# Kernel optimization log

Hardware: AMD Instinct MI355X
Metric: run time of the kernel (lower is better)

The kernel has to match this reference:

```python
import jax, jax.numpy as jnp
import numpy as np

G = 4096              # number of graphs in batch
NPG = 198             # nodes per graph (fixed by view(-1, 198*2))
N = G * NPG           # total nodes = 811008
DEG = 8               # avg degree
E = N * DEG           # total edges = 6488064
CONV_DIMS = [(2, 20), (20, 15), (15, 10), (10, 5), (5, 2)]
MLP_DIMS = [(396, 200), (200, 100), (100, 50), (50, 10), (10, 2)]


def setup_inputs() -> dict:
    key = jax.random.key(0)
    ks = jax.random.split(key, 64)
    x = jax.random.normal(ks[0], (N, 2), dtype=jnp.float32)
    # block-diagonal edges: endpoints within each 198-node graph, then offset
    src = jax.random.randint(ks[1], (G, E // G), 0, NPG)
    dst = jax.random.randint(ks[2], (G, E // G), 0, NPG)
    off = (jnp.arange(G, dtype=jnp.int32) * NPG)[:, None]
    edge_index = jnp.stack([(src + off).reshape(-1), (dst + off).reshape(-1)]).astype(jnp.int32)
    edge_weight = jax.random.uniform(ks[3], (E,), dtype=jnp.float32)
    inp = {"x": x, "edge_index": edge_index, "edge_weight": edge_weight}
    ki = 4
    for i, (ci, co) in enumerate(CONV_DIMS):
        s = 1.0 / np.sqrt(ci)
        inp[f"w_rel{i}"] = jax.random.normal(ks[ki], (co, ci), jnp.float32) * s; ki += 1
        inp[f"b_rel{i}"] = jax.random.normal(ks[ki], (co,), jnp.float32) * s; ki += 1
        inp[f"w_root{i}"] = jax.random.normal(ks[ki], (co, ci), jnp.float32) * s; ki += 1
    for i, (ci, co) in enumerate(MLP_DIMS):
        s = 1.0 / np.sqrt(ci)
        inp[f"lw{i}"] = jax.random.normal(ks[ki], (co, ci), jnp.float32) * s; ki += 1
        inp[f"lb{i}"] = jax.random.normal(ks[ki], (co,), jnp.float32) * s; ki += 1
    return inp


def _graph_conv(x, src, dst, ew, w_rel, b_rel, w_root):
    # PyG GraphConv: lin_rel(sum_{j->i} e_ji * x_j) + lin_root(x_i)
    msg = x[src] * ew[:, None]                               # [E, Cin] gather
    agg = jax.ops.segment_sum(msg, dst, num_segments=N)      # [N, Cin] scatter-add
    return agg @ w_rel.T + b_rel + x @ w_root.T              # [N, Cout]


def reference(x, edge_index, edge_weight,
              w_rel0, b_rel0, w_root0, w_rel1, b_rel1, w_root1,
              w_rel2, b_rel2, w_root2, w_rel3, b_rel3, w_root3,
              w_rel4, b_rel4, w_root4,
              lw0, lb0, lw1, lb1, lw2, lb2, lw3, lb3, lw4, lb4):
    src, dst = edge_index[0], edge_index[1]
    convs = [(w_rel0, b_rel0, w_root0), (w_rel1, b_rel1, w_root1),
             (w_rel2, b_rel2, w_root2), (w_rel3, b_rel3, w_root3),
             (w_rel4, b_rel4, w_root4)]
    h = x
    for wr, br, wroot in convs:
        h = jax.nn.relu(_graph_conv(h, src, dst, edge_weight, wr, br, wroot))
    h = h.reshape(-1, NPG * 2)                               # [G, 396]
    mlp = [(lw0, lb0), (lw1, lb1), (lw2, lb2), (lw3, lb3)]
    for w, b in mlp:
        h = jax.nn.relu(h @ w.T + b)
    logits = h @ lw4.T + lb4                                 # [G, 2]
    return jax.nn.softmax(logits, axis=1)
```

## Files before the change

### kernel.cpp

```cpp
#include <hip/hip_runtime.h>
#include <hip/hip_fp16.h>

#define NG    4096
#define NPG   198
#define EPG   1584
#define ETOT  (NG * EPG)
#define SWW   14

#define BC2(u) __builtin_bit_cast(__half2, (u))

typedef _Float16 f16x4 __attribute__((ext_vector_type(4)));
typedef float    f32x4 __attribute__((ext_vector_type(4)));
typedef float    f32x2 __attribute__((ext_vector_type(2)));

#define H_F16S    (NG * 396)
#define WTB_SZ    114688
#define WTB1_OFF  83200
#define WTB2_OFF  106496
#define WTB3_OFF  113664
#define CPK_PAIRS 562

__global__ __launch_bounds__(256) void wpack_kernel(
    const float* __restrict__ w0, const float* __restrict__ w1,
    const float* __restrict__ w2, const float* __restrict__ w3,
    const float* wr0, const float* wq0, const float* wr1, const float* wq1,
    const float* wr2, const float* wq2, const float* wr3, const float* wq3,
    const float* wr4, const float* wq4,
    _Float16* __restrict__ wtb, f32x2* __restrict__ cpk)
{
    const int idx = blockIdx.x * 256 + threadIdx.x;
    if (idx < 2 * WTB_SZ) {
        const int half = idx >= WTB_SZ;
        const int rel0 = idx - half * WTB_SZ;
        const float* w; int K, N, NPAD, rel;
        if (rel0 < 83200)       { w = w0; K = 396; N = 200; NPAD = 208; rel = rel0; }
        else if (rel0 < 106496) { w = w1; K = 200; N = 100; NPAD = 112; rel = rel0 - 83200; }
        else if (rel0 < 113664) { w = w2; K = 100; N = 50;  NPAD = 64;  rel = rel0 - 106496; }
        else                    { w = w3; K = 50;  N = 10;  NPAD = 16;  rel = rel0 - 113664; }
        const int span = NPAD * 16;
        const int kc = rel / span;
        const int r  = rel - kc * span;
        const int n  = r >> 4, ki = r & 15;
        const int k  = kc * 16 + ki;
        const float v = (n < N && k < K) ? w[n * K + k] : 0.f;
        const _Float16 hi = (_Float16)v;
        wtb[idx] = half ? (_Float16)(v - (float)hi) : hi;
        return;
    }
    const int cidx = idx - 2 * WTB_SZ;
    if (cidx >= CPK_PAIRS) return;
    const float *wrel, *wroot; int COUT, CIN, MSP, base;
    if (cidx < 40)       { wrel=wr0; wroot=wq0; COUT=20; CIN=2;  MSP=1;  base=0;   }
    else if (cidx < 340) { wrel=wr1; wroot=wq1; COUT=15; CIN=20; MSP=10; base=40;  }
    else if (cidx < 500) { wrel=wr2; wroot=wq2; COUT=10; CIN=15; MSP=8;  base=340; }
    else if (cidx < 550) { wrel=wr3; wroot=wq3; COUT=5;  CIN=10; MSP=5;  base=500; }
    else                 { wrel=wr4; wroot=wq4; COUT=2;  CIN=5;  MSP=3;  base=550; }
    const int r    = cidx - base;
    const int half = r >= COUT * MSP;
    const int q    = r - half * COUT * MSP;
    const int o    = q / MSP, p = q - o * MSP;
    const float* w = half ? wroot : wrel;
    const int c0 = 2 * p, c1 = 2 * p + 1;
    f32x2 v;
    v.x = (c0 < CIN) ? w[o * CIN + c0] : 0.f;
    v.y = (c1 < CIN) ? w[o * CIN + c1] : 0.f;
    cpk[cidx] = v;
}

template <int CIN, int COUT, int SIN, int SOUT>
__device__ __forceinline__ void conv_layer_h(
    const unsigned* __restrict__ h_in,
    unsigned* __restrict__ h_out,
    const unsigned* __restrict__ s_edge,
    const unsigned short* __restrict__ row_start,
    const unsigned short* __restrict__ perm,
    const f32x2* __restrict__ wrelp,
    const f32x2* __restrict__ wrootp,
    const float* __restrict__ brel, int tid)
{
    if (tid >= NPG) return;
    const int node = (int)perm[tid];
    constexpr int MS = (CIN + 1) / 2;

    float aggf[MS * 2];
#pragma unroll
    for (int c = 0; c < MS * 2; ++c) aggf[c] = 0.f;

    const unsigned jb = row_start[node], je = row_start[node + 1];
    for (unsigned j = jb; j < je; ++j) {
        const unsigned e  = s_edge[j];
        const float    wf = __half2float(__ushort_as_half((unsigned short)(e >> 16)));
        const unsigned* row = h_in + (e & 0xFFFFu) * SIN;
        unsigned wv[MS];
        if constexpr (SIN == 1) {
            wv[0] = row[0];
        } else {
#pragma unroll
            for (int p = 0; p + 1 < MS; p += 2) {
                const uint2 q = *(const uint2*)(row + p);
                wv[p] = q.x; wv[p + 1] = q.y;
            }
            if constexpr (MS & 1) wv[MS - 1] = row[MS - 1];
        }
#pragma unroll
        for (int p = 0; p < MS; ++p) {
            const __half2 h2 = BC2(wv[p]);
            aggf[2*p]     = fmaf(wf, __low2float(h2),  aggf[2*p]);
            aggf[2*p + 1] = fmaf(wf, __high2float(h2), aggf[2*p + 1]);
        }
    }

    float hv[MS * 2];
    {
        const unsigned* me = h_in + node * SIN;
        unsigned mw[MS];
        if constexpr (SIN == 1) {
            mw[0] = me[0];
        } else {
#pragma unroll
            for (int p = 0; p + 1 < MS; p += 2) {
                const uint2 q = *(const uint2*)(me + p);
                mw[p] = q.x; mw[p + 1] = q.y;
            }
            if constexpr (MS & 1) mw[MS - 1] = me[MS - 1];
        }
#pragma unroll
        for (int p = 0; p < MS; ++p) {
            const __half2 h2 = BC2(mw[p]);
            hv[2*p]     = __low2float(h2);
            hv[2*p + 1] = __high2float(h2);
        }
    }

    float outv[COUT];
#pragma unroll
    for (int o = 0; o < COUT; ++o) {
        f32x2 acc; acc.x = brel[o]; acc.y = 0.f;
#pragma unroll
        for (int p = 0; p < MS; ++p) {
            f32x2 av; av.x = aggf[2*p]; av.y = aggf[2*p+1];
            acc = __builtin_elementwise_fma(av, wrelp[o * MS + p], acc);
            f32x2 hv2; hv2.x = hv[2*p]; hv2.y = hv[2*p+1];
            acc = __builtin_elementwise_fma(hv2, wrootp[o * MS + p], acc);
        }
        outv[o] = fmaxf(acc.x + acc.y, 0.f);
    }

    if constexpr (SOUT == 1) {
        h_out[node] = __builtin_bit_cast(unsigned,
            __floats2half2_rn(outv[0], COUT > 1 ? outv[1] : 0.f));
    } else {
        unsigned ow[SOUT];
#pragma unroll
        for (int p = 0; p < SOUT; ++p) {
            const float lo = (2 * p     < COUT) ? outv[2 * p]     : 0.f;
            const float hi = (2 * p + 1 < COUT) ? outv[2 * p + 1] : 0.f;
            ow[p] = __builtin_bit_cast(unsigned, __floats2half2_rn(lo, hi));
        }
        unsigned* orow = h_out + node * SOUT;
#pragma unroll
        for (int qn = 0; qn < SOUT; qn += 2)
            *(uint2*)(orow + qn) = make_uint2(ow[qn], ow[qn + 1]);
    }
}

__global__ __launch_bounds__(256) void conv_kernel(
    const float* __restrict__ x,
    const int*   __restrict__ eidx,
    const float* __restrict__ ew,
    const f32x2* __restrict__ cpk,
    const float* __restrict__ br0, const float* __restrict__ br1,
    const float* __restrict__ br2, const float* __restrict__ br3,
    const float* __restrict__ br4,
    _Float16* __restrict__ H)
{
    __shared__ __align__(16) unsigned s_edge[EPG];
    __shared__ unsigned       cnt[256];
    __shared__ unsigned short row_start[NPG + 2];
    __shared__ unsigned       wsum[4];
    __shared__ unsigned       dhist[64];
    __shared__ unsigned       dcur[64];
    __shared__ unsigned short perm[NPG + 2];
    __shared__ __align__(16) unsigned bufA[NPG * SWW];
    __shared__ __align__(16) unsigned bufB[NPG * SWW];

    const int g = blockIdx.x, tid = threadIdx.x;
    const int ebase = g * EPG, nbase = g * NPG;
    const int lane = tid & 63, wid = tid >> 6;

    const int4*   s4 = (const int4*)(eidx + ebase);
    const int4*   d4 = (const int4*)(eidx + ETOT + ebase);
    const float4* w4 = (const float4*)(ew + ebase);
    const int4   sa = s4[tid];
    const int4   da = d4[tid];
    const float4 wa = w4[tid];
    const bool hasb = tid < (EPG / 4 - 256);
    int4 sb = {0,0,0,0}, db = {0,0,0,0}; float4 wb = {0,0,0,0};
    if (hasb) { sb = s4[tid + 256]; db = d4[tid + 256]; wb = w4[tid + 256]; }

    cnt[tid] = 0u;
    __syncthreads();
    atomicAdd(&cnt[da.x - nbase], 1u); atomicAdd(&cnt[da.y - nbase], 1u);
    atomicAdd(&cnt[da.z - nbase], 1u); atomicAdd(&cnt[da.w - nbase], 1u);
    if (hasb) {
        atomicAdd(&cnt[db.x - nbase], 1u); atomicAdd(&cnt[db.y - nbase], 1u);
        atomicAdd(&cnt[db.z - nbase], 1u); atomicAdd(&cnt[db.w - nbase], 1u);
    }
    __syncthreads();

    const unsigned v = cnt[tid];
    unsigned inc = v;
#pragma unroll
    for (int s = 1; s < 64; s <<= 1) {
        const unsigned t = (unsigned)__shfl_up((int)inc, s);
        if (lane >= s) inc += t;
    }
    if (lane == 63) wsum[wid] = inc;
    __syncthreads();
    unsigned pre = 0;
    for (int w = 0; w < wid; ++w) pre += wsum[w];
    const unsigned excl = pre + inc - v;
    if (tid <= NPG) row_start[tid] = (unsigned short)excl;
    cnt[tid] = excl;
    __syncthreads();

    {
        auto place = [&](int s, int d, float w) {
            const int dl = d - nbase;
            const unsigned slot = atomicAdd(&cnt[dl], 1u);
            const __half hw = __float2half_rn(w);
            s_edge[slot] = ((unsigned)__half_as_ushort(hw) << 16)
                         | (unsigned)(s - nbase);
        };
        place(sa.x, da.x, wa.x); place(sa.y, da.y, wa.y);
        place(sa.z, da.z, wa.z); place(sa.w, da.w, wa.w);
        if (hasb) {
            place(sb.x, db.x, wb.x); place(sb.y, db.y, wb.y);
            place(sb.z, db.z, wb.z); place(sb.w, db.w, wb.w);
        }
    }

    if (tid < NPG) {
        const float2 xv = ((const float2*)x)[nbase + tid];
        bufA[tid] = __builtin_bit_cast(unsigned, __floats2half2_rn(xv.x, xv.y));
    }

    if (tid < 64) dhist[tid] = 0u;
    __syncthreads();
    unsigned mydeg = 0u;
    if (tid < NPG) {
        mydeg = v; if (mydeg > 63u) mydeg = 63u;
        atomicAdd(&dhist[mydeg], 1u);
    }
    __syncthreads();
    if (tid < 64) {
        const unsigned dv = dhist[tid];
        unsigned sc = dv;
#pragma unroll
        for (int s = 1; s < 64; s <<= 1) {
            const unsigned t = (unsigned)__shfl_up((int)sc, s);
            if (lane >= s) sc += t;
        }
        dcur[tid] = sc - dv;
    }
    __syncthreads();
    if (tid < NPG) {
        const unsigned pos = atomicAdd(&dcur[mydeg], 1u);
        perm[pos] = (unsigned short)tid;
    }
    __syncthreads();

    conv_layer_h<2,  20, 1,   SWW>(bufA, bufB, s_edge, row_start, perm,
                                   cpk + 0,   cpk + 20,        br0, tid);
    __syncthreads();
    conv_layer_h<20, 15, SWW, SWW>(bufB, bufA, s_edge, row_start, perm,
                                   cpk + 40,  cpk + 40 + 150,  br1, tid);
    __syncthreads();
    conv_layer_h<15, 10, SWW, SWW>(bufA, bufB, s_edge, row_start, perm,
                                   cpk + 340, cpk + 340 + 80,  br2, tid);
    __syncthreads();
    conv_layer_h<10, 5,  SWW, SWW>(bufB, bufA, s_edge, row_start, perm,
                                   cpk + 500, cpk + 500 + 25,  br3, tid);
    __syncthreads();
    conv_layer_h<5,  2,  SWW, 1  >(bufA, bufB, s_edge, row_start, perm,
                                   cpk + 550, cpk + 550 + 6,   br4, tid);
    __syncthreads();

    if (tid < NPG)
        ((unsigned*)H)[g * NPG + tid] = bufB[tid];
}

__device__ __forceinline__ void zero_words(void* p, int nwords, int tid)
{
    unsigned* u = (unsigned*)p;
    for (int i = tid; i < nwords; i += 512) u[i] = 0u;
}

template<int KC, int NTT, int NOUT, int SIN, int SOUT>
__device__ __forceinline__ void mfma_layer(
    const _Float16* __restrict__ inb,
    _Float16* __restrict__ outb,
    const _Float16* __restrict__ wthi,
    const _Float16* __restrict__ wtlo,
    const float* __restrict__ bias, int tid)
{
    constexpr int NPAD = NTT * 16;
    const int lane = tid & 63, wid = tid >> 6;
    const int lrow = lane & 15, lgrp = lane >> 4;
    const int nt0 = wid;
    if (nt0 >= NTT) return;
    const bool has2 = (nt0 + 8) < NTT;
    const _Float16* aptr = inb + lrow * SIN + lgrp * 4;

    f32x4 acc0 = {0.f, 0.f, 0.f, 0.f};
    f32x4 acc1 = {0.f, 0.f, 0.f, 0.f};
    const int n0 = nt0 * 16 + lrow;
    const int n1 = (nt0 + 8) * 16 + lrow;
    const int boff0 = n0 * 16 + lgrp * 4;
    const int boff1 = n1 * 16 + lgrp * 4;
#pragma unroll 4
    for (int kc = 0; kc < KC; ++kc) {
        const f16x4 a = *(const f16x4*)(aptr + kc * 16);
        const size_t kb = (size_t)kc * (NPAD * 16);
        acc0 = __builtin_amdgcn_mfma_f32_16x16x16f16(
            a, *(const f16x4*)(wthi + kb + boff0), acc0, 0, 0, 0);
        acc0 = __builtin_amdgcn_mfma_f32_16x16x16f16(
            a, *(const f16x4*)(wtlo + kb + boff0), acc0, 0, 0, 0);
        if (has2) {
            acc1 = __builtin_amdgcn_mfma_f32_16x16x16f16(
                a, *(const f16x4*)(wthi + kb + boff1), acc1, 0, 0, 0);
            acc1 = __builtin_amdgcn_mfma_f32_16x16x16f16(
                a, *(const f16x4*)(wtlo + kb + boff1), acc1, 0, 0, 0);
        }
    }
    if (n0 < NOUT) {
        const float bv = bias[n0];
#pragma unroll
        for (int j = 0; j < 4; ++j)
            outb[(lgrp * 4 + j) * SOUT + n0] = (_Float16)fmaxf(acc0[j] + bv, 0.f);
    }
    if (has2 && n1 < NOUT) {
        const float bv = bias[n1];
#pragma unroll
        for (int j = 0; j < 4; ++j)
            outb[(lgrp * 4 + j) * SOUT + n1] = (_Float16)fmaxf(acc1[j] + bv, 0.f);
    }
}

__global__ __launch_bounds__(512) void mlp_mfma_kernel(
    const _Float16* __restrict__ H,
    const _Float16* __restrict__ wtb,
    const float* __restrict__ lb0, const float* __restrict__ lb1,
    const float* __restrict__ lb2, const float* __restrict__ lb3,
    const float* __restrict__ lw4, const float* __restrict__ lb4,
    float* __restrict__ out)
{
    __shared__ __align__(16) _Float16 bufH[16 * 400];
    __shared__ __align__(16) _Float16 bufX[16 * 224];
    __shared__ __align__(16) _Float16 bufY[16 * 128];

    const int tid   = threadIdx.x;
    const int gbase = blockIdx.x * 8;
    const _Float16* lo = wtb + WTB_SZ;

    {
        const unsigned* Hw = (const unsigned*)H + (size_t)gbase * 198;
        unsigned* bH = (unsigned*)bufH;
        for (int t = tid; t < 16 * 200; t += 512) {
            const int gg = t / 200, w = t - gg * 200;
            bH[gg * 200 + w] = (gg < 8 && w < 198) ? Hw[gg * 198 + w] : 0u;
        }
        zero_words(bufX, 16 * 224 / 2, tid);
        zero_words(bufY, 16 * 128 / 2, tid);
    }
    __syncthreads();

    mfma_layer<25, 13, 200, 400, 224>(bufH, bufX, wtb, lo, lb0, tid);
    __syncthreads();

    zero_words(bufH, 512, tid);
    mfma_layer<13, 7, 100, 224, 128>(bufX, bufY, wtb + WTB1_OFF, lo + WTB1_OFF, lb1, tid);
    __syncthreads();

    zero_words(bufX, 128, tid);
    mfma_layer<7, 4, 50, 128, 64>(bufY, bufH, wtb + WTB2_OFF, lo + WTB2_OFF, lb2, tid);
    __syncthreads();

    mfma_layer<4, 1, 10, 64, 16>(bufH, bufX, wtb + WTB3_OFF, lo + WTB3_OFF, lb3, tid);
    __syncthreads();

    if (tid < 8) {
        float l0 = lb4[0], l1 = lb4[1];
#pragma unroll
        for (int k = 0; k < 10; ++k) {
            const float hv = (float)bufX[tid * 16 + k];
            l0 = fmaf(hv, lw4[k],      l0);
            l1 = fmaf(hv, lw4[10 + k], l1);
        }
        const float m  = fmaxf(l0, l1);
        const float e0 = __expf(l0 - m), e1 = __expf(l1 - m);
        const float inv = 1.f / (e0 + e1);
        float2 p; p.x = e0 * inv; p.y = e1 * inv;
        ((float2*)out)[gbase + tid] = p;
    }
}

extern "C" void kernel_launch(void* const* d_in, const int* in_sizes, int n_in,
                              void* d_out, int out_size, void* d_ws, size_t ws_size,
                              hipStream_t stream)
{
    const float* x    = (const float*)d_in[0];
    const int*   eidx = (const int*)  d_in[1];
    const float* ew   = (const float*)d_in[2];

    const float* wr[5]; const float* br[5]; const float* wq[5];
    for (int i = 0; i < 5; ++i) {
        wr[i] = (const float*)d_in[3 + 3 * i];
        br[i] = (const float*)d_in[4 + 3 * i];
        wq[i] = (const float*)d_in[5 + 3 * i];
    }
    const float* lw[5]; const float* lb[5];
    for (int i = 0; i < 5; ++i) {
        lw[i] = (const float*)d_in[18 + 2 * i];
        lb[i] = (const float*)d_in[19 + 2 * i];
    }

    _Float16* wsH = (_Float16*)d_ws;
    _Float16* wtb = wsH + (size_t)H_F16S;
    f32x2*    cpk = (f32x2*)(wtb + (size_t)(2 * WTB_SZ));

    const int total_pack = 2 * WTB_SZ + CPK_PAIRS;
    wpack_kernel<<<(total_pack + 255) / 256, 256, 0, stream>>>(
        lw[0], lw[1], lw[2], lw[3],
        wr[0], wq[0], wr[1], wq[1], wr[2], wq[2], wr[3], wq[3], wr[4], wq[4],
        wtb, cpk);

    conv_kernel<<<NG, 256, 0, stream>>>(
        x, eidx, ew, cpk,
        br[0], br[1], br[2], br[3], br[4],
        wsH);

    mlp_mfma_kernel<<<NG / 8, 512, 0, stream>>>(
        wsH, wtb,
        lb[0], lb[1], lb[2], lb[3],
        lw[4], lb[4],
        (float*)d_out);
}
```

Measured before the change: 121.5 us.

## Split each graph node across two threads in the fused GraphConv kernel

The conv kernel now launches 512 threads per graph instead of 256, and each node is handled by a pair of threads. The two threads split the node's incoming edges, combine partial aggregates with a lane shuffle, and then each computes half of the output channels. The shared feature stride drops from 14 to 12 words, and neighbour rows are read as 16-byte loads. Edge loading also changes to one int4 group per thread. The aim is more parallelism on the latency-bound gather and transform stages, at the cost of a larger block, a shuffle reduction, and uneven output halves.

```diff
diff --git a/kernel.cpp b/kernel.cpp
--- a/kernel.cpp
+++ b/kernel.cpp
@@ -5,7 +5,7 @@
 #define NPG   198
 #define EPG   1584
 #define ETOT  (NG * EPG)
-#define SWW   14
+#define SHW   12
 
 #define BC2(u) __builtin_bit_cast(__half2, (u))
 
@@ -68,7 +68,7 @@
 }
 
 template <int CIN, int COUT, int SIN, int SOUT>
-__device__ __forceinline__ void conv_layer_h(
+__device__ __forceinline__ void conv_layer_pair(
     const unsigned* __restrict__ h_in,
     unsigned* __restrict__ h_out,
     const unsigned* __restrict__ s_edge,
@@ -78,37 +78,61 @@
     const f32x2* __restrict__ wrootp,
     const float* __restrict__ brel, int tid)
 {
-    if (tid >= NPG) return;
-    const int node = (int)perm[tid];
-    constexpr int MS = (CIN + 1) / 2;
+    if (tid >= 2 * NPG) return;
+    const int node = (int)perm[tid >> 1];
+    const int half = tid & 1;
+    constexpr int MS   = (CIN + 1) / 2;
+    constexpr int SPL  = (COUT / 2 + 1) & ~1;
+    constexpr int NH1  = COUT - SPL;
+    constexpr int MAXO = (SPL > NH1) ? SPL : NH1;
 
     float aggf[MS * 2];
 #pragma unroll
     for (int c = 0; c < MS * 2; ++c) aggf[c] = 0.f;
 
-    const unsigned jb = row_start[node], je = row_start[node + 1];
-    for (unsigned j = jb; j < je; ++j) {
-        const unsigned e  = s_edge[j];
-        const float    wf = __half2float(__ushort_as_half((unsigned short)(e >> 16)));
-        const unsigned* row = h_in + (e & 0xFFFFu) * SIN;
-        unsigned wv[MS];
-        if constexpr (SIN == 1) {
-            wv[0] = row[0];
-        } else {
-#pragma unroll
-            for (int p = 0; p + 1 < MS; p += 2) {
-                const uint2 q = *(const uint2*)(row + p);
-                wv[p] = q.x; wv[p + 1] = q.y;
+    {
+        const unsigned jb0 = row_start[node], je0 = row_start[node + 1];
+        const unsigned mid = jb0 + ((je0 - jb0 + 1) >> 1);
+        const unsigned jb = half ? mid : jb0;
+        const unsigned je = half ? je0 : mid;
+        for (unsigned j = jb; j < je; ++j) {
+            const unsigned e  = s_edge[j];
+            const float    wf = __half2float(__ushort_as_half((unsigned short)(e >> 16)));
+            const unsigned* row = h_in + (e & 0xFFFFu) * SIN;
+            unsigned wv[MS];
+            if constexpr (SIN == 1) {
+                wv[0] = row[0];
+            } else {
+                const uint4 q0 = *(const uint4*)row;
+                wv[0] = q0.x;
+                if constexpr (MS > 1) wv[1] = q0.y;
+                if constexpr (MS > 2) wv[2] = q0.z;
+                if constexpr (MS > 3) wv[3] = q0.w;
+                if constexpr (MS > 4) {
+                    const uint4 q1 = *(const uint4*)(row + 4);
+                    wv[4] = q1.x;
+                    if constexpr (MS > 5) wv[5] = q1.y;
+                    if constexpr (MS > 6) wv[6] = q1.z;
+                    if constexpr (MS > 7) wv[7] = q1.w;
+                }
+                if constexpr (MS > 8) {
+                    const uint4 q2 = *(const uint4*)(row + 8);
+                    wv[8] = q2.x;
+                    if constexpr (MS > 9) wv[9] = q2.y;
+                }
             }
-            if constexpr (MS & 1) wv[MS - 1] = row[MS - 1];
-        }
-#pragma unroll
-        for (int p = 0; p < MS; ++p) {
-            const __half2 h2 = BC2(wv[p]);
-            aggf[2*p]     = fmaf(wf, __low2float(h2),  aggf[2*p]);
-            aggf[2*p + 1] = fmaf(wf, __high2float(h2), aggf[2*p + 1]);
-        }
-    }
+#pragma unroll
+            for (int p = 0; p < MS; ++p) {
+                const __half2 h2 = BC2(wv[p]);
+                aggf[2*p]     = fmaf(wf, __low2float(h2),  aggf[2*p]);
+                aggf[2*p + 1] = fmaf(wf, __high2float(h2), aggf[2*p + 1]);
+            }
+        }
+    }
+
+#pragma unroll
+    for (int c = 0; c < MS * 2; ++c)
+        aggf[c] += __shfl_xor(aggf[c], 1);
 
     float hv[MS * 2];
     {
@@ -117,12 +141,23 @@
         if constexpr (SIN == 1) {
             mw[0] = me[0];
         } else {
-#pragma unroll
-            for (int p = 0; p + 1 < MS; p += 2) {
-                const uint2 q = *(const uint2*)(me + p);
-                mw[p] = q.x; mw[p + 1] = q.y;
+            const uint4 q0 = *(const uint4*)me;
+            mw[0] = q0.x;
+            if constexpr (MS > 1) mw[1] = q0.y;
+            if constexpr (MS > 2) mw[2] = q0.z;
+            if constexpr (MS > 3) mw[3] = q0.w;
+            if constexpr (MS > 4) {
+                const uint4 q1 = *(const uint4*)(me + 4);
+                mw[4] = q1.x;
+                if constexpr (MS > 5) mw[5] = q1.y;
+                if constexpr (MS > 6) mw[6] = q1.z;
+                if constexpr (MS > 7) mw[7] = q1.w;
             }
-            if constexpr (MS & 1) mw[MS - 1] = me[MS - 1];
+            if constexpr (MS > 8) {
+                const uint4 q2 = *(const uint4*)(me + 8);
+                mw[8] = q2.x;
+                if constexpr (MS > 9) mw[9] = q2.y;
+            }
         }
 #pragma unroll
         for (int p = 0; p < MS; ++p) {
@@ -132,39 +167,43 @@
         }
     }
 
-    float outv[COUT];
-#pragma unroll
-    for (int o = 0; o < COUT; ++o) {
-        f32x2 acc; acc.x = brel[o]; acc.y = 0.f;
-#pragma unroll
-        for (int p = 0; p < MS; ++p) {
-            f32x2 av; av.x = aggf[2*p]; av.y = aggf[2*p+1];
-            acc = __builtin_elementwise_fma(av, wrelp[o * MS + p], acc);
-            f32x2 hv2; hv2.x = hv[2*p]; hv2.y = hv[2*p+1];
-            acc = __builtin_elementwise_fma(hv2, wrootp[o * MS + p], acc);
-        }
-        outv[o] = fmaxf(acc.x + acc.y, 0.f);
-    }
-
-    if constexpr (SOUT == 1) {
-        h_out[node] = __builtin_bit_cast(unsigned,
-            __floats2half2_rn(outv[0], COUT > 1 ? outv[1] : 0.f));
+    float outv[MAXO];
+    const int nout  = half ? NH1 : SPL;
+    const int obase = half ? SPL : 0;
+#pragma unroll
+    for (int i = 0; i < MAXO; ++i) {
+        if (i < nout) {
+            const int o = obase + i;
+            f32x2 acc; acc.x = brel[o]; acc.y = 0.f;
+#pragma unroll
+            for (int p = 0; p < MS; ++p) {
+                f32x2 av;  av.x  = aggf[2*p]; av.y  = aggf[2*p+1];
+                acc = __builtin_elementwise_fma(av,  wrelp[o * MS + p], acc);
+                f32x2 hv2; hv2.x = hv[2*p];   hv2.y = hv[2*p+1];
+                acc = __builtin_elementwise_fma(hv2, wrootp[o * MS + p], acc);
+            }
+            outv[i] = fmaxf(acc.x + acc.y, 0.f);
+        }
+    }
+
+    unsigned* orow = h_out + node * SOUT;
+    if (half == 0) {
+#pragma unroll
+        for (int w = 0; w < SPL / 2; ++w)
+            orow[w] = __builtin_bit_cast(unsigned,
+                __floats2half2_rn(outv[2*w], outv[2*w+1]));
     } else {
-        unsigned ow[SOUT];
-#pragma unroll
-        for (int p = 0; p < SOUT; ++p) {
-            const float lo = (2 * p     < COUT) ? outv[2 * p]     : 0.f;
-            const float hi = (2 * p + 1 < COUT) ? outv[2 * p + 1] : 0.f;
-            ow[p] = __builtin_bit_cast(unsigned, __floats2half2_rn(lo, hi));
-        }
-        unsigned* orow = h_out + node * SOUT;
-#pragma unroll
-        for (int qn = 0; qn < SOUT; qn += 2)
-            *(uint2*)(orow + qn) = make_uint2(ow[qn], ow[qn + 1]);
-    }
-}
-
-__global__ __launch_bounds__(256) void conv_kernel(
+#pragma unroll
+        for (int w = SPL / 2; w < SOUT; ++w) {
+            const int i = 2 * w - SPL;
+            const float lo = (i     < NH1) ? outv[i]     : 0.f;
+            const float hi = (i + 1 < NH1) ? outv[i + 1] : 0.f;
+            orow[w] = __builtin_bit_cast(unsigned, __floats2half2_rn(lo, hi));
+        }
+    }
+}
+
+__global__ __launch_bounds__(512) void conv_kernel(
     const float* __restrict__ x,
     const int*   __restrict__ eidx,
     const float* __restrict__ ew,
@@ -181,8 +220,8 @@
     __shared__ unsigned       dhist[64];
     __shared__ unsigned       dcur[64];
     __shared__ unsigned short perm[NPG + 2];
-    __shared__ __align__(16) unsigned bufA[NPG * SWW];
-    __shared__ __align__(16) unsigned bufB[NPG * SWW];
+    __shared__ __align__(16) unsigned bufA[NPG * SHW];
+    __shared__ __align__(16) unsigned bufB[NPG * SHW];
 
     const int g = blockIdx.x, tid = threadIdx.x;
     const int ebase = g * EPG, nbase = g * NPG;
@@ -191,40 +230,40 @@
     const int4*   s4 = (const int4*)(eidx + ebase);
     const int4*   d4 = (const int4*)(eidx + ETOT + ebase);
     const float4* w4 = (const float4*)(ew + ebase);
-    const int4   sa = s4[tid];
-    const int4   da = d4[tid];
-    const float4 wa = w4[tid];
-    const bool hasb = tid < (EPG / 4 - 256);
-    int4 sb = {0,0,0,0}, db = {0,0,0,0}; float4 wb = {0,0,0,0};
-    if (hasb) { sb = s4[tid + 256]; db = d4[tid + 256]; wb = w4[tid + 256]; }
-
-    cnt[tid] = 0u;
-    __syncthreads();
-    atomicAdd(&cnt[da.x - nbase], 1u); atomicAdd(&cnt[da.y - nbase], 1u);
-    atomicAdd(&cnt[da.z - nbase], 1u); atomicAdd(&cnt[da.w - nbase], 1u);
-    if (hasb) {
-        atomicAdd(&cnt[db.x - nbase], 1u); atomicAdd(&cnt[db.y - nbase], 1u);
-        atomicAdd(&cnt[db.z - nbase], 1u); atomicAdd(&cnt[db.w - nbase], 1u);
-    }
-    __syncthreads();
-
-    const unsigned v = cnt[tid];
-    unsigned inc = v;
-#pragma unroll
-    for (int s = 1; s < 64; s <<= 1) {
-        const unsigned t = (unsigned)__shfl_up((int)inc, s);
-        if (lane >= s) inc += t;
-    }
-    if (lane == 63) wsum[wid] = inc;
-    __syncthreads();
-    unsigned pre = 0;
-    for (int w = 0; w < wid; ++w) pre += wsum[w];
-    const unsigned excl = pre + inc - v;
-    if (tid <= NPG) row_start[tid] = (unsigned short)excl;
-    cnt[tid] = excl;
-    __syncthreads();
-
-    {
+    const bool havq = tid < (EPG / 4);
+    int4 sa = {0,0,0,0}, da = {0,0,0,0}; float4 wa = {0,0,0,0};
+    if (havq) { sa = s4[tid]; da = d4[tid]; wa = w4[tid]; }
+
+    if (tid < 256) cnt[tid] = 0u;
+    __syncthreads();
+    if (havq) {
+        atomicAdd(&cnt[da.x - nbase], 1u); atomicAdd(&cnt[da.y - nbase], 1u);
+        atomicAdd(&cnt[da.z - nbase], 1u); atomicAdd(&cnt[da.w - nbase], 1u);
+    }
+    __syncthreads();
+
+    unsigned v = 0;
+    if (tid < 256) {
+        v = cnt[tid];
+        unsigned inc = v;
+#pragma unroll
+        for (int s = 1; s < 64; s <<= 1) {
+            const unsigned t = (unsigned)__shfl_up((int)inc, s);
+            if (lane >= s) inc += t;
+        }
+        if (lane == 63) wsum[wid] = inc;
+        __syncthreads();
+        unsigned pre = 0;
+        for (int w = 0; w < wid; ++w) pre += wsum[w];
+        const unsigned excl = pre + inc - v;
+        if (tid <= NPG) row_start[tid] = (unsigned short)excl;
+        cnt[tid] = excl;
+    } else {
+        __syncthreads();
+    }
+    __syncthreads();
+
+    if (havq) {
         auto place = [&](int s, int d, float w) {
             const int dl = d - nbase;
             const unsigned slot = atomicAdd(&cnt[dl], 1u);
@@ -234,10 +273,6 @@
         };
         place(sa.x, da.x, wa.x); place(sa.y, da.y, wa.y);
         place(sa.z, da.z, wa.z); place(sa.w, da.w, wa.w);
-        if (hasb) {
-            place(sb.x, db.x, wb.x); place(sb.y, db.y, wb.y);
-            place(sb.z, db.z, wb.z); place(sb.w, db.w, wb.w);
-        }
     }
 
     if (tid < NPG) {
@@ -270,20 +305,20 @@
     }
     __syncthreads();
 
-    conv_layer_h<2,  20, 1,   SWW>(bufA, bufB, s_edge, row_start, perm,
-                                   cpk + 0,   cpk + 20,        br0, tid);
-    __syncthreads();
-    conv_layer_h<20, 15, SWW, SWW>(bufB, bufA, s_edge, row_start, perm,
-                                   cpk + 40,  cpk + 40 + 150,  br1, tid);
-    __syncthreads();
-    conv_layer_h<15, 10, SWW, SWW>(bufA, bufB, s_edge, row_start, perm,
-                                   cpk + 340, cpk + 340 + 80,  br2, tid);
-    __syncthreads();
-    conv_layer_h<10, 5,  SWW, SWW>(bufB, bufA, s_edge, row_start, perm,
-                                   cpk + 500, cpk + 500 + 25,  br3, tid);
-    __syncthreads();
-    conv_layer_h<5,  2,  SWW, 1  >(bufA, bufB, s_edge, row_start, perm,
-                                   cpk + 550, cpk + 550 + 6,   br4, tid);
+    conv_layer_pair<2,  20, 1,   SHW>(bufA, bufB, s_edge, row_start, perm,
+                                      cpk + 0,   cpk + 20,        br0, tid);
+    __syncthreads();
+    conv_layer_pair<20, 15, SHW, SHW>(bufB, bufA, s_edge, row_start, perm,
+                                      cpk + 40,  cpk + 40 + 150,  br1, tid);
+    __syncthreads();
+    conv_layer_pair<15, 10, SHW, SHW>(bufA, bufB, s_edge, row_start, perm,
+                                      cpk + 340, cpk + 340 + 80,  br2, tid);
+    __syncthreads();
+    conv_layer_pair<10, 5,  SHW, SHW>(bufB, bufA, s_edge, row_start, perm,
+                                      cpk + 500, cpk + 500 + 25,  br3, tid);
+    __syncthreads();
+    conv_layer_pair<5,  2,  SHW, 1  >(bufA, bufB, s_edge, row_start, perm,
+                                      cpk + 550, cpk + 550 + 6,   br4, tid);
     __syncthreads();
 
     if (tid < NPG)
@@ -435,7 +470,7 @@
         wr[0], wq[0], wr[1], wq[1], wr[2], wq[2], wr[3], wq[3], wr[4], wq[4],
         wtb, cpk);
 
-    conv_kernel<<<NG, 256, 0, stream>>>(
+    conv_kernel<<<NG, 512, 0, stream>>>(
         x, eidx, ew, cpk,
         br[0], br[1], br[2], br[3], br[4],
         wsH);
```

After: 467.9 us. +285.1%, slower.
